# Kernel optimization log

Hardware: AMD Instinct MI355X
Metric: run time of the kernel (lower is better)

The kernel has to match this reference:

```python
import jax, jax.numpy as jnp
import numpy as np

EMBED = 1024
HEADS = 16
HEAD_DIM = EMBED // HEADS
HIDDEN = 4 * EMBED
EPS = 1e-5


def setup_inputs() -> dict:
    key = jax.random.key(0)
    ks = jax.random.split(key, 9)
    s = lambda fan_in: 1.0 / np.sqrt(fan_in)
    inp = {
        "x": jax.random.normal(ks[0], (2, 2048, EMBED), dtype=jnp.float32),
        "ln1_w": jnp.ones((EMBED,), jnp.float32),
        "ln1_b": jnp.zeros((EMBED,), jnp.float32),
        "ln2_w": jnp.ones((EMBED,), jnp.float32),
        "ln2_b": jnp.zeros((EMBED,), jnp.float32),
        "qkv_w": jax.random.uniform(ks[1], (EMBED, 3 * EMBED), jnp.float32, -s(EMBED), s(EMBED)),
        "qkv_b": jax.random.uniform(ks[2], (3 * EMBED,), jnp.float32, -s(EMBED), s(EMBED)),
        "proj_w": jax.random.uniform(ks[3], (EMBED, EMBED), jnp.float32, -s(EMBED), s(EMBED)),
        "proj_b": jax.random.uniform(ks[4], (EMBED,), jnp.float32, -s(EMBED), s(EMBED)),
        "fc1_w": jax.random.uniform(ks[5], (EMBED, HIDDEN), jnp.float32, -s(EMBED), s(EMBED)),
        "fc1_b": jax.random.uniform(ks[6], (HIDDEN,), jnp.float32, -s(EMBED), s(EMBED)),
        "fc2_w": jax.random.uniform(ks[7], (HIDDEN, EMBED), jnp.float32, -s(HIDDEN), s(HIDDEN)),
        "fc2_b": jax.random.uniform(ks[8], (EMBED,), jnp.float32, -s(HIDDEN), s(HIDDEN)),
    }
    return inp


def _layernorm(x, w, b):
    mu = jnp.mean(x, axis=-1, keepdims=True)
    var = jnp.mean(jnp.square(x - mu), axis=-1, keepdims=True)
    return (x - mu) * jax.lax.rsqrt(var + EPS) * w + b


def _attn(x, qkv_w, qkv_b, proj_w, proj_b):
    B, N, C = x.shape
    qkv = x @ qkv_w + qkv_b                      # [B,N,3C]
    qkv = qkv.reshape(B, N, 3, HEADS, HEAD_DIM)
    q, k, v = qkv[:, :, 0], qkv[:, :, 1], qkv[:, :, 2]   # [B,N,H,D]
    scale = HEAD_DIM ** -0.5
    scores = jnp.einsum("bqhd,bkhd->bhqk", q, k) * scale  # [B,H,N,N]
    attn = jax.nn.softmax(scores, axis=-1)
    out = jnp.einsum("bhqk,bkhd->bqhd", attn, v).reshape(B, N, C)
    return out @ proj_w + proj_b


def _mlp(x, fc1_w, fc1_b, fc2_w, fc2_b):
    h = jax.nn.gelu(x @ fc1_w + fc1_b, approximate=False)
    return h @ fc2_w + fc2_b


def reference(x, ln1_w, ln1_b, ln2_w, ln2_b, qkv_w, qkv_b, proj_w, proj_b,
              fc1_w, fc1_b, fc2_w, fc2_b):
    # pre-norm transformer block (eval mode: dropout/drop_path are identity)
    x = x + _attn(_layernorm(x, ln1_w, ln1_b), qkv_w, qkv_b, proj_w, proj_b)
    x = x + _mlp(_layernorm(x, ln2_w, ln2_b), fc1_w, fc1_b, fc2_w, fc2_b)
    return x
```

## Files before the change

kernel.cpp:

```cpp
#include <hip/hip_runtime.h>
#include <hip/hip_bf16.h>

#define SEQ    2048
#define BATCH  2
#define MTOK   4096
#define EMBED  1024
#define HEADS  16
#define HDIM   64
#define QKV3   3072
#define FFN    4096

typedef __attribute__((ext_vector_type(8))) short bf16x8;
typedef __attribute__((ext_vector_type(4))) float f32x4;
typedef __attribute__((ext_vector_type(16))) float f32x16;

static __device__ __forceinline__ unsigned short f2bf(float f) {
  union { float f; unsigned u; } x; x.f = f;
  unsigned r = x.u + 0x7FFFu + ((x.u >> 16) & 1u);
  return (unsigned short)(r >> 16);
}
static __device__ __forceinline__ float bf2f(unsigned short u) {
  union { unsigned u; float f; } x; x.u = ((unsigned)u) << 16; return x.f;
}
static __device__ __forceinline__ unsigned pk2bf(float a, float b) {
#if __has_builtin(__builtin_amdgcn_cvt_pk_bf16_f32)
  typedef __attribute__((ext_vector_type(2))) __bf16 bf16x2_t;
  union { bf16x2_t v; unsigned u; } x;
  x.v = __builtin_amdgcn_cvt_pk_bf16_f32(a, b);
  return x.u;
#else
  return ((unsigned)f2bf(a)) | (((unsigned)f2bf(b)) << 16);
#endif
}
static __device__ __forceinline__ float fexp2(float x) {
#if __has_builtin(__builtin_amdgcn_exp2f)
  return __builtin_amdgcn_exp2f(x);
#else
  return exp2f(x);
#endif
}
static __device__ __forceinline__ float frcp(float x) {
#if __has_builtin(__builtin_amdgcn_rcpf)
  return __builtin_amdgcn_rcpf(x);
#else
  return 1.0f / x;
#endif
}
static __device__ __forceinline__ float fgelu(float v) {
  float t = v * v;
  float z = v * __builtin_fmaf(-0.1029456f, t, -2.3022650687f);
  return v * frcp(1.0f + fexp2(z));
}

static __device__ __forceinline__ void halfswap(unsigned a, unsigned b, int hi,
                                                unsigned& lo_out, unsigned& hi_out) {
#if __has_builtin(__builtin_amdgcn_permlane32_swap)
  typedef __attribute__((ext_vector_type(2))) unsigned uint2v;
  uint2v r = __builtin_amdgcn_permlane32_swap(a, b, false, false);
  lo_out = r[0];
  hi_out = r[1];
#else
  unsigned as = (unsigned)__shfl_xor((int)a, 32);
  unsigned bs = (unsigned)__shfl_xor((int)b, 32);
  lo_out = hi ? bs : a;
  hi_out = hi ? b : as;
#endif
}

static __device__ __forceinline__ void gload16(const unsigned short* g, unsigned short* l) {
  __builtin_amdgcn_global_load_lds((const __attribute__((address_space(1))) void*)g,
                                   (__attribute__((address_space(3))) void*)l, 16, 0, 0);
}

struct TD { const float* W; unsigned short* T; int K, N, ntx, base; };
struct TD4 { TD d[4]; };

__global__ void transpose_all(TD4 td) {
  __shared__ float t[32][33];
  int bid = blockIdx.x;
  int i = 0;
  if (bid >= td.d[1].base) i = 1;
  if (bid >= td.d[2].base) i = 2;
  if (bid >= td.d[3].base) i = 3;
  const TD& D = td.d[i];
  int local = bid - D.base;
  int n0 = (local % D.ntx) * 32, k0 = (local / D.ntx) * 32;
  int tx = threadIdx.x, ty = threadIdx.y;
#pragma unroll
  for (int j = 0; j < 32; j += 8)
    t[ty + j][tx] = D.W[(size_t)(k0 + ty + j) * D.N + n0 + tx];
  __syncthreads();
#pragma unroll
  for (int j = 0; j < 32; j += 8)
    D.T[(size_t)(n0 + ty + j) * D.K + k0 + tx] = f2bf(t[tx][ty + j]);
}

__global__ __launch_bounds__(256) void ln_kernel(const float* __restrict__ in,
                                                 const float* __restrict__ w,
                                                 const float* __restrict__ b,
                                                 unsigned short* __restrict__ out) {
  __shared__ float sh[4];
  int row = blockIdx.x, tid = threadIdx.x;
  const float4 v = ((const float4*)(in + (size_t)row * EMBED))[tid];
  float s = v.x + v.y + v.z + v.w;
#pragma unroll
  for (int off = 32; off; off >>= 1) s += __shfl_xor(s, off);
  if ((tid & 63) == 0) sh[tid >> 6] = s;
  __syncthreads();
  float mean = (sh[0] + sh[1] + sh[2] + sh[3]) * (1.0f / EMBED);
  __syncthreads();
  float dx = v.x - mean, dy = v.y - mean, dz = v.z - mean, dw = v.w - mean;
  float q = dx * dx + dy * dy + dz * dz + dw * dw;
#pragma unroll
  for (int off = 32; off; off >>= 1) q += __shfl_xor(q, off);
  if ((tid & 63) == 0) sh[tid >> 6] = q;
  __syncthreads();
  float var = (sh[0] + sh[1] + sh[2] + sh[3]) * (1.0f / EMBED);
  float rs = rsqrtf(var + 1e-5f);
  const float4 wv = ((const float4*)w)[tid];
  const float4 bv = ((const float4*)b)[tid];
  ushort4 o;
  o.x = f2bf(dx * rs * wv.x + bv.x);
  o.y = f2bf(dy * rs * wv.y + bv.y);
  o.z = f2bf(dz * rs * wv.z + bv.z);
  o.w = f2bf(dw * rs * wv.w + bv.w);
  ((ushort4*)(out + (size_t)row * EMBED))[tid] = o;
}

template <int ACT, int OUTBF, int VSPLIT>
__global__ __launch_bounds__(256) void gemmBig(const unsigned short* __restrict__ A,
                                               const unsigned short* __restrict__ Wt,
                                               const float* __restrict__ bias,
                                               unsigned short* __restrict__ outB,
                                               float* __restrict__ outF,
                                               unsigned short* __restrict__ vT,
                                               int M, int N, int K, int nblk) {
  __shared__ __align__(16) unsigned short As[128 * 64];
  __shared__ __align__(16) unsigned short Bs[128 * 64];
  const int tid = threadIdx.x;
  const int wave = tid >> 6, lane = tid & 63;
  const int quad = lane >> 4, ml = lane & 15;
  const int wr = wave >> 1, wc = wave & 1;
  const int m0 = (blockIdx.x / nblk) * 128;
  const int n0 = (blockIdx.x % nblk) * 128;
  const int srow = lane >> 3;
  const int schunk = (lane & 7) ^ (srow & 7);
  const unsigned short* Ag = A + (size_t)(m0 + wave * 32 + srow) * K + schunk * 8;
  const unsigned short* Bg = Wt + (size_t)(n0 + wave * 32 + srow) * K + schunk * 8;
  unsigned short* AsW = &As[wave * 2048];
  unsigned short* BsW = &Bs[wave * 2048];
  f32x4 acc[4][4];
#pragma unroll
  for (int i = 0; i < 4; i++)
#pragma unroll
    for (int j = 0; j < 4; j++) acc[i][j] = (f32x4){0.f, 0.f, 0.f, 0.f};
  for (int k0 = 0; k0 < K; k0 += 64) {
    __syncthreads();
#pragma unroll
    for (int t = 0; t < 4; t++) {
      gload16(Ag + (size_t)(8 * t) * K, AsW + 512 * t);
      gload16(Bg + (size_t)(8 * t) * K, BsW + 512 * t);
    }
    Ag += 64; Bg += 64;
    __syncthreads();
#pragma unroll
    for (int kh = 0; kh < 2; kh++) {
      const int ch = ((kh * 4 + quad) ^ (ml & 7)) * 8;
      bf16x8 af[4], bfr[4];
#pragma unroll
      for (int mt = 0; mt < 4; mt++)
        af[mt] = *(const bf16x8*)&As[(wr * 64 + mt * 16 + ml) * 64 + ch];
#pragma unroll
      for (int nt = 0; nt < 4; nt++)
        bfr[nt] = *(const bf16x8*)&Bs[(wc * 64 + nt * 16 + ml) * 64 + ch];
#pragma unroll
      for (int mt = 0; mt < 4; mt++)
#pragma unroll
        for (int nt = 0; nt < 4; nt++)
          acc[mt][nt] = __builtin_amdgcn_mfma_f32_16x16x32_bf16(af[mt], bfr[nt], acc[mt][nt], 0, 0, 0);
    }
  }
#pragma unroll
  for (int mt = 0; mt < 4; mt++)
#pragma unroll
    for (int nt = 0; nt < 4; nt++) {
      const int col0 = n0 + wc * 64 + nt * 16;
      const int row0 = m0 + wr * 64 + mt * 16;
      if (VSPLIT && col0 >= 2 * EMBED) {
        const int b = row0 >> 11, tok0 = row0 & (SEQ - 1);
        const int h = (col0 - 2 * EMBED) >> 6;
        const int dl = ((col0 - 2 * EMBED) & 63) + ml;
        float bia = bias[col0 + ml];
        ushort4 o;
        o.x = f2bf(acc[mt][nt][0] + bia);
        o.y = f2bf(acc[mt][nt][1] + bia);
        o.z = f2bf(acc[mt][nt][2] + bia);
        o.w = f2bf(acc[mt][nt][3] + bia);
        *(ushort4*)(vT + (size_t)((b * 16 + h) * 64 + dl) * SEQ + tok0 + quad * 4) = o;
      } else {
#pragma unroll
        for (int r = 0; r < 4; r++) {
          int row = row0 + quad * 4 + r;
          int col = col0 + ml;
          float v = acc[mt][nt][r] + bias[col];
          if (ACT) v = fgelu(v);
          if (OUTBF)
            outB[(size_t)row * N + col] = f2bf(v);
          else
            outF[(size_t)row * N + col] = v;
        }
      }
    }
}

template <int RES, int OUTBF>
__global__ __launch_bounds__(256) void gemm64k(const unsigned short* __restrict__ A,
                                               const unsigned short* __restrict__ Wt,
                                               const float* __restrict__ bias,
                                               const float* __restrict__ res,
                                               unsigned short* __restrict__ outB,
                                               float* __restrict__ outF,
                                               int M, int N, int K, int nblk) {
  __shared__ __align__(16) unsigned short As[2][128 * 64];
  __shared__ __align__(16) unsigned short Bs[2][64 * 64];
  const int tid = threadIdx.x;
  const int wave = tid >> 6, lane = tid & 63;
  const int quad = lane >> 4, ml = lane & 15;
  const int wr = wave >> 1, wc = wave & 1;
  const int xcd = blockIdx.x & 7, idx = blockIdx.x >> 3;
  const int mPerXcd = (gridDim.x >> 3) / nblk;
  const int m0 = (xcd * mPerXcd + idx / nblk) * 128;
  const int n0 = (idx % nblk) * 64;
  const int srow = lane >> 3;
  const int schunk = (lane & 7) ^ (srow & 7);
  const unsigned short* Ag = A + (size_t)(m0 + wave * 32 + srow) * K + schunk * 8;
  const unsigned short* Bg = Wt + (size_t)(n0 + wave * 16 + srow) * K + schunk * 8;
  f32x4 acc[4][2];
#pragma unroll
  for (int i = 0; i < 4; i++) { acc[i][0] = (f32x4){0.f,0.f,0.f,0.f}; acc[i][1] = acc[i][0]; }
  {
    unsigned short* AsW = &As[0][wave * 2048];
    unsigned short* BsW = &Bs[0][wave * 1024];
    gload16(Ag, AsW);
    gload16(Ag + (size_t)8 * K,  AsW + 512);
    gload16(Ag + (size_t)16 * K, AsW + 1024);
    gload16(Ag + (size_t)24 * K, AsW + 1536);
    gload16(Bg, BsW);
    gload16(Bg + (size_t)8 * K,  BsW + 512);
    Ag += 64; Bg += 64;
  }
  __syncthreads();
  const int nk = K >> 6;
  for (int kk = 0; kk < nk; ++kk) {
    const int cur = kk & 1;
    if (kk + 1 < nk) {
      unsigned short* AsW = &As[cur ^ 1][wave * 2048];
      unsigned short* BsW = &Bs[cur ^ 1][wave * 1024];
      gload16(Ag, AsW);
      gload16(Ag + (size_t)8 * K,  AsW + 512);
      gload16(Ag + (size_t)16 * K, AsW + 1024);
      gload16(Ag + (size_t)24 * K, AsW + 1536);
      gload16(Bg, BsW);
      gload16(Bg + (size_t)8 * K,  BsW + 512);
      Ag += 64; Bg += 64;
    }
#pragma unroll
    for (int kh = 0; kh < 2; kh++) {
      const int ch = ((kh * 4 + quad) ^ (ml & 7)) * 8;
      bf16x8 af[4], bfr[2];
#pragma unroll
      for (int mt = 0; mt < 4; mt++)
        af[mt] = *(const bf16x8*)&As[cur][(wr * 64 + mt * 16 + ml) * 64 + ch];
#pragma unroll
      for (int nt = 0; nt < 2; nt++)
        bfr[nt] = *(const bf16x8*)&Bs[cur][(wc * 32 + nt * 16 + ml) * 64 + ch];
#pragma unroll
      for (int mt = 0; mt < 4; mt++)
#pragma unroll
        for (int nt = 0; nt < 2; nt++)
          acc[mt][nt] = __builtin_amdgcn_mfma_f32_16x16x32_bf16(af[mt], bfr[nt], acc[mt][nt], 0, 0, 0);
    }
    __syncthreads();
  }
#pragma unroll
  for (int mt = 0; mt < 4; mt++)
#pragma unroll
    for (int nt = 0; nt < 2; nt++)
#pragma unroll
      for (int r = 0; r < 4; r++) {
        int row = m0 + wr * 64 + mt * 16 + quad * 4 + r;
        int col = n0 + wc * 32 + nt * 16 + ml;
        float v = acc[mt][nt][r] + bias[col];
        if (RES) v += res[(size_t)row * N + col];
        if (OUTBF)
          outB[(size_t)row * N + col] = f2bf(v);
        else
          outF[(size_t)row * N + col] = v;
      }
}

__global__ __launch_bounds__(256, 4) void attn_kernel(const unsigned short* __restrict__ qkv,
                                                      const unsigned short* __restrict__ vT,
                                                      unsigned short* __restrict__ attn) {
  __shared__ __align__(16) unsigned short Ks[2][64 * 64];
  __shared__ __align__(16) unsigned short Vs[2][64 * 64];
  const int tid = threadIdx.x, wave = tid >> 6, lane = tid & 63;
  const int l31 = lane & 31, hi = lane >> 5;
  const int qs = wave & 1, kh = wave >> 1;
  const int bh = blockIdx.x, b = bh >> 4, h = bh & 15;
  const int q0w = blockIdx.y * 64 + qs * 32;
  const float qscale = 0.18033688011112042f;
  const int sw = l31 & 7;

  const unsigned short* qrow = qkv + (size_t)(b * SEQ + q0w + l31) * QKV3 + h * HDIM;
  bf16x8 bq[4];
#pragma unroll
  for (int s = 0; s < 4; s++) {
    bq[s] = *(const bf16x8*)(qrow + s * 16 + hi * 8);
#pragma unroll
    for (int j = 0; j < 8; j++)
      bq[s][j] = (short)f2bf(bf2f((unsigned short)bq[s][j]) * qscale);
  }
  bf16x8 ones;
#pragma unroll
  for (int j = 0; j < 8; j++) ones[j] = (short)0x3F80;

  f32x16 zz;
#pragma unroll
  for (int i = 0; i < 16; i++) zz[i] = 0.f;
  f32x16 O0 = zz, O1 = zz, lsum = zz;

  const int skey = lane >> 3;
  const int schunk8 = ((lane & 7) ^ (skey & 7)) * 8;
  const unsigned short* kbase =
      qkv + (size_t)(b * SEQ + wave * 16 + skey) * QKV3 + EMBED + h * HDIM + schunk8;
  const unsigned short* vbase =
      vT + (size_t)(bh * 64 + wave * 16 + skey) * SEQ + schunk8;

  gload16(kbase, &Ks[0][wave * 1024]);
  gload16(kbase + (size_t)8 * QKV3, &Ks[0][wave * 1024] + 512);
  gload16(vbase, &Vs[0][wave * 1024]);
  gload16(vbase + (size_t)8 * SEQ, &Vs[0][wave * 1024] + 512);
  __syncthreads();

  const int krow0 = kh * 32;
  for (int kti = 0; kti < SEQ / 64; ++kti) {
    const int cur = kti & 1;
    if (kti + 1 < SEQ / 64) {
      const int kt = (kti + 1) * 64;
      unsigned short* kd = &Ks[cur ^ 1][wave * 1024];
      unsigned short* vd = &Vs[cur ^ 1][wave * 1024];
      gload16(kbase + (size_t)kt * QKV3, kd);
      gload16(kbase + (size_t)(kt + 8) * QKV3, kd + 512);
      gload16(vbase + kt, vd);
      gload16(vbase + kt + (size_t)8 * SEQ, vd + 512);
    }
    const unsigned short* Kc = &Ks[cur][0];
    const unsigned short* Vc = &Vs[cur][0];

    f32x16 St = zz;
#pragma unroll
    for (int s = 0; s < 4; s++) {
      bf16x8 ak = *(const bf16x8*)&Kc[(krow0 + l31) * 64 + ((2 * s + hi) ^ sw) * 8];
      St = __builtin_amdgcn_mfma_f32_32x32x16_bf16(ak, bq[s], St, 0, 0, 0);
    }

    unsigned W0[4], W1[4];
#pragma unroll
    for (int g = 0; g < 4; g++) {
      W0[g] = pk2bf(fexp2(St[4 * g]), fexp2(St[4 * g + 1]));
      W1[g] = pk2bf(fexp2(St[4 * g + 2]), fexp2(St[4 * g + 3]));
    }

    bf16x8 pa[2];
#pragma unroll
    for (int ks = 0; ks < 2; ks++) {
      const int g0 = 2 * ks, g1 = g0 + 1;
      unsigned w0, w1, w2, w3;
      halfswap(W0[g0], W0[g1], hi, w0, w2);
      halfswap(W1[g0], W1[g1], hi, w1, w3);
      union { unsigned u[4]; bf16x8 v; } pw;
      pw.u[0] = w0; pw.u[1] = w1; pw.u[2] = w2; pw.u[3] = w3;
      pa[ks] = pw.v;
    }

    __builtin_amdgcn_s_setprio(1);
    lsum = __builtin_amdgcn_mfma_f32_32x32x16_bf16(pa[0], ones, lsum, 0, 0, 0);
    lsum = __builtin_amdgcn_mfma_f32_32x32x16_bf16(pa[1], ones, lsum, 0, 0, 0);
#pragma unroll
    for (int ks = 0; ks < 2; ks++) {
      const int ch = kh * 4 + ks * 2 + hi;
      bf16x8 bv0 = *(const bf16x8*)&Vc[l31 * 64 + (ch ^ sw) * 8];
      bf16x8 bv1 = *(const bf16x8*)&Vc[(32 + l31) * 64 + (ch ^ sw) * 8];
      O0 = __builtin_amdgcn_mfma_f32_32x32x16_bf16(pa[ks], bv0, O0, 0, 0, 0);
      O1 = __builtin_amdgcn_mfma_f32_32x32x16_bf16(pa[ks], bv1, O1, 0, 0, 0);
    }
    __builtin_amdgcn_s_setprio(0);
    __syncthreads();
  }

  if (kh == 1) {
    float* sc = qs ? (float*)&Vs[0][0] : (float*)&Ks[0][0];
#pragma unroll
    for (int r = 0; r < 16; r++) {
      sc[lane * 48 + r]      = lsum[r];
      sc[lane * 48 + 16 + r] = O0[r];
      sc[lane * 48 + 32 + r] = O1[r];
    }
  }
  __syncthreads();
  if (kh == 0) {
    const float* sc = qs ? (const float*)&Vs[0][0] : (const float*)&Ks[0][0];
#pragma unroll
    for (int r = 0; r < 16; r++) {
      lsum[r] += sc[lane * 48 + r];
      O0[r]   += sc[lane * 48 + 16 + r];
      O1[r]   += sc[lane * 48 + 32 + r];
    }
#pragma unroll
    for (int r = 0; r < 16; r++) {
      const int qr = (r & 3) + 8 * (r >> 2) + 4 * hi;
      float inv = 1.0f / lsum[r];
      size_t g = (size_t)(b * SEQ + q0w + qr) * EMBED + h * HDIM + l31;
      attn[g]      = f2bf(O0[r] * inv);
      attn[g + 32] = f2bf(O1[r] * inv);
    }
  }
}

extern "C" void kernel_launch(void* const* d_in, const int* in_sizes, int n_in,
                              void* d_out, int out_size, void* d_ws, size_t ws_size,
                              hipStream_t stream) {
  const float* x      = (const float*)d_in[0];
  const float* ln1_w  = (const float*)d_in[1];
  const float* ln1_b  = (const float*)d_in[2];
  const float* ln2_w  = (const float*)d_in[3];
  const float* ln2_b  = (const float*)d_in[4];
  const float* qkv_w  = (const float*)d_in[5];
  const float* qkv_b  = (const float*)d_in[6];
  const float* proj_w = (const float*)d_in[7];
  const float* proj_b = (const float*)d_in[8];
  const float* fc1_w  = (const float*)d_in[9];
  const float* fc1_b  = (const float*)d_in[10];
  const float* fc2_w  = (const float*)d_in[11];
  const float* fc2_b  = (const float*)d_in[12];
  float* out = (float*)d_out;
  char* wsb = (char*)d_ws;
  unsigned short* lnbuf  = (unsigned short*)(wsb + 0);
  unsigned short* qkvb   = (unsigned short*)(wsb + 8388608);
  unsigned short* attnb  = (unsigned short*)(wsb + 33554432);
  unsigned short* vTb    = (unsigned short*)(wsb + 41943040);
  unsigned short* actb   = (unsigned short*)(wsb + 33554432);
  float*          h1     = (float*)(wsb + 67108864);
  unsigned short* qkvWt  = (unsigned short*)(wsb + 83886080);
  unsigned short* projWt = (unsigned short*)(wsb + 90177536);
  unsigned short* fc1Wt  = (unsigned short*)(wsb + 92274688);
  unsigned short* fc2Wt  = (unsigned short*)(wsb + 100663296);

  TD4 td;
  td.d[0] = {qkv_w,  qkvWt,  1024, 3072,  96, 0};
  td.d[1] = {proj_w, projWt, 1024, 1024,  32, 3072};
  td.d[2] = {fc1_w,  fc1Wt,  1024, 4096, 128, 4096};
  td.d[3] = {fc2_w,  fc2Wt,  4096, 1024,  32, 8192};
  transpose_all<<<12288, dim3(32, 8), 0, stream>>>(td);

  ln_kernel<<<MTOK, 256, 0, stream>>>(x, ln1_w, ln1_b, lnbuf);
  gemmBig<0, 1, 1><<<768, 256, 0, stream>>>(
      lnbuf, qkvWt, qkv_b, qkvb, nullptr, vTb, MTOK, QKV3, EMBED, 24);
  attn_kernel<<<dim3(32, 32), 256, 0, stream>>>(qkvb, vTb, attnb);
  gemm64k<1, 0><<<512, 256, 0, stream>>>(
      attnb, projWt, proj_b, x, nullptr, h1, MTOK, EMBED, EMBED, 16);
  ln_kernel<<<MTOK, 256, 0, stream>>>(h1, ln2_w, ln2_b, lnbuf);
  gemmBig<1, 1, 0><<<1024, 256, 0, stream>>>(
      lnbuf, fc1Wt, fc1_b, actb, nullptr, nullptr, MTOK, FFN, EMBED, 32);
  gemm64k<1, 0><<<512, 256, 0, stream>>>(
      actb, fc2Wt, fc2_b, h1, nullptr, out, MTOK, EMBED, FFN, 16);
}
```

Baseline: 343.5 us.

## Add 256x256-tile 8-wave GEMM kernel with phased staging for fc1+GELU

Adds a new gemm256 kernel that uses 256x256 output tiles with 512 threads and double-buffered LDS filled through global_load_lds. Each K step is split into four phases, interleaving async loads with MFMA work under barriers and s_setprio. The fc1 GEMM with GELU now uses it in place of gemmBig. The larger tiles increase operand reuse but cut the grid to 256 blocks, which is about one wave of work across the CUs, and use 128KB of LDS per block, so occupancy drops.

```diff
diff --git a/kernel.cpp b/kernel.cpp
--- a/kernel.cpp
+++ b/kernel.cpp
@@ -71,6 +71,8 @@
   __builtin_amdgcn_global_load_lds((const __attribute__((address_space(1))) void*)g,
                                    (__attribute__((address_space(3))) void*)l, 16, 0, 0);
 }
+
+#define MEMFENCE asm volatile("" ::: "memory")
 
 struct TD { const float* W; unsigned short* T; int K, N, ntx, base; };
 struct TD4 { TD d[4]; };
@@ -211,6 +213,117 @@
         }
       }
     }
+}
+
+__global__ __launch_bounds__(512, 2) void gemm256(const unsigned short* __restrict__ A,
+                                                  const unsigned short* __restrict__ Wt,
+                                                  const float* __restrict__ bias,
+                                                  unsigned short* __restrict__ outB,
+                                                  int M, int N, int K, int nblk) {
+  __shared__ __align__(16) unsigned short As[2][256 * 64];
+  __shared__ __align__(16) unsigned short Bs[2][256 * 64];
+  const int tid = threadIdx.x;
+  const int wave = tid >> 6, lane = tid & 63;
+  const int quad = lane >> 4, ml = lane & 15;
+  const int wr = wave >> 2, wc = wave & 3;
+  const int m0 = (blockIdx.x / nblk) * 256;
+  const int n0 = (blockIdx.x % nblk) * 256;
+  const int srow = lane >> 3;
+  const int schunk = (lane & 7) ^ (srow & 7);
+  const unsigned short* Ag = A  + (size_t)(m0 + wave * 32 + srow) * K + schunk * 8;
+  const unsigned short* Bg = Wt + (size_t)(n0 + wave * 32 + srow) * K + schunk * 8;
+  f32x4 acc[8][4];
+#pragma unroll
+  for (int i = 0; i < 8; i++)
+#pragma unroll
+    for (int j = 0; j < 4; j++) acc[i][j] = (f32x4){0.f, 0.f, 0.f, 0.f};
+
+#pragma unroll
+  for (int g = 0; g < 4; g++) {
+    gload16(Ag + (size_t)(g * 8) * K, &As[0][(wave * 32 + g * 8) * 64]);
+    gload16(Bg + (size_t)(g * 8) * K, &Bs[0][(wave * 32 + g * 8) * 64]);
+  }
+
+  const int nit = K >> 7;
+  for (int it = 0; it < nit; ++it) {
+#pragma unroll
+    for (int half = 0; half < 2; ++half) {
+      const int rs = half;
+      const int ss = half ^ 1;
+      const int kst = 2 * it + 1 + half;
+      const bool doStage = (kst < 2 * nit);
+      const unsigned short* Asl = &As[rs][0];
+      const unsigned short* Bsl = &Bs[rs][0];
+      bf16x8 bfr[4][2];
+#pragma unroll
+      for (int ph = 0; ph < 4; ++ph) {
+        bf16x8 af[2][2];
+        if (ph > 0) {
+#pragma unroll
+          for (int mt2 = 0; mt2 < 2; ++mt2)
+#pragma unroll
+            for (int kk = 0; kk < 2; ++kk)
+              af[mt2][kk] = *(const bf16x8*)&Asl[(wr * 128 + (ph * 2 + mt2) * 16 + ml) * 64 +
+                                                ((kk * 4 + quad) ^ (ml & 7)) * 8];
+        }
+        if (doStage) {
+          if (ph < 2) {
+            gload16(Ag + (size_t)((ph * 2) * 8) * K + kst * 64,
+                    &As[ss][(wave * 32 + (ph * 2) * 8) * 64]);
+            gload16(Ag + (size_t)((ph * 2 + 1) * 8) * K + kst * 64,
+                    &As[ss][(wave * 32 + (ph * 2 + 1) * 8) * 64]);
+          } else {
+            gload16(Bg + (size_t)(((ph - 2) * 2) * 8) * K + kst * 64,
+                    &Bs[ss][(wave * 32 + ((ph - 2) * 2) * 8) * 64]);
+            gload16(Bg + (size_t)(((ph - 2) * 2 + 1) * 8) * K + kst * 64,
+                    &Bs[ss][(wave * 32 + ((ph - 2) * 2 + 1) * 8) * 64]);
+          }
+        }
+        if (ph == 0) {
+          if (doStage) { asm volatile("s_waitcnt vmcnt(2)" ::: "memory"); }
+          else         { asm volatile("s_waitcnt vmcnt(0)" ::: "memory"); }
+          MEMFENCE; __builtin_amdgcn_s_barrier(); MEMFENCE;
+#pragma unroll
+          for (int nt = 0; nt < 4; ++nt)
+#pragma unroll
+            for (int kk = 0; kk < 2; ++kk)
+              bfr[nt][kk] = *(const bf16x8*)&Bsl[(wc * 64 + nt * 16 + ml) * 64 +
+                                                ((kk * 4 + quad) ^ (ml & 7)) * 8];
+#pragma unroll
+          for (int mt2 = 0; mt2 < 2; ++mt2)
+#pragma unroll
+            for (int kk = 0; kk < 2; ++kk)
+              af[mt2][kk] = *(const bf16x8*)&Asl[(wr * 128 + mt2 * 16 + ml) * 64 +
+                                                ((kk * 4 + quad) ^ (ml & 7)) * 8];
+        } else {
+          MEMFENCE; __builtin_amdgcn_s_barrier(); MEMFENCE;
+        }
+        __builtin_amdgcn_s_setprio(1);
+#pragma unroll
+        for (int mt2 = 0; mt2 < 2; ++mt2)
+#pragma unroll
+          for (int nt = 0; nt < 4; ++nt)
+#pragma unroll
+            for (int kk = 0; kk < 2; ++kk)
+              acc[ph * 2 + mt2][nt] = __builtin_amdgcn_mfma_f32_16x16x32_bf16(
+                  af[mt2][kk], bfr[nt][kk], acc[ph * 2 + mt2][nt], 0, 0, 0);
+        __builtin_amdgcn_s_setprio(0);
+        MEMFENCE; __builtin_amdgcn_s_barrier(); MEMFENCE;
+      }
+    }
+  }
+#pragma unroll
+  for (int mt = 0; mt < 8; ++mt)
+#pragma unroll
+    for (int nt = 0; nt < 4; ++nt)
+#pragma unroll
+      for (int r = 0; r < 4; ++r) {
+        int row = m0 + wr * 128 + mt * 16 + quad * 4 + r;
+        int col = n0 + wc * 64 + nt * 16 + ml;
+        float v = acc[mt][nt][r] + bias[col];
+        v = fgelu(v);
+        outB[(size_t)row * N + col] = f2bf(v);
+      }
 }
 
 template <int RES, int OUTBF>
@@ -471,8 +584,8 @@
   gemm64k<1, 0><<<512, 256, 0, stream>>>(
       attnb, projWt, proj_b, x, nullptr, h1, MTOK, EMBED, EMBED, 16);
   ln_kernel<<<MTOK, 256, 0, stream>>>(h1, ln2_w, ln2_b, lnbuf);
-  gemmBig<1, 1, 0><<<1024, 256, 0, stream>>>(
-      lnbuf, fc1Wt, fc1_b, actb, nullptr, nullptr, MTOK, FFN, EMBED, 32);
+  gemm256<<<256, 512, 0, stream>>>(
+      lnbuf, fc1Wt, fc1_b, actb, MTOK, FFN, EMBED, 16);
   gemm64k<1, 0><<<512, 256, 0, stream>>>(
       actb, fc2Wt, fc2_b, h1, nullptr, out, MTOK, EMBED, FFN, 16);
 }
```

Result: no change. 339.5 us (-1.2%).
